# Optimization experiments

Measured on AMD Instinct MI355X. Metric: run time of the kernel, lower is better.

## Reference

```python
import jax, jax.numpy as jnp
import numpy as np


def setup_inputs() -> dict:
    key = jax.random.key(0)
    k1, k2 = jax.random.split(key)
    B, D, K = 8192, 4096, 16
    x = jax.random.normal(k1, (B, D), dtype=jnp.float32)
    # kaiming_uniform_(a=sqrt(5)) on [K, D]: bound = sqrt(6/((1+5)*fan_in)) = 1/sqrt(D)
    bound = 1.0 / np.sqrt(D)
    w = jax.random.uniform(k2, (K, D), dtype=jnp.float32, minval=-bound, maxval=bound)
    return {"x": x, "w": w}


def reference(x, w):
    # z[b,d] = x[b,d] * (1 + sum_{i=1..k} w[i-1,d] * x[b,(d+i) mod D])
    k = w.shape[0]
    acc = jnp.ones_like(x)
    for i in range(1, k + 1):
        acc = acc + w[i - 1][None, :] * jnp.roll(x, -i, axis=1)
    return x * acc
```

## Files before the change

kernel.cpp:

```cpp
#include <hip/hip_runtime.h>


#define D 4096
#define DG 1024
#define K 16
#define TPB 256
#define TILE_B 8
#define ROW_F4 260
#define ROW_F (ROW_F4 * 4)

__global__ __launch_bounds__(TPB) void quad_enhancer_kernel(
    const float* __restrict__ x, const float* __restrict__ w,
    float* __restrict__ out) {
  __shared__ float lds[TILE_B * ROW_F];

  const int tid = threadIdx.x;
  const int cg0 = blockIdx.x * TPB;
  const int cg = cg0 + tid;
  const int b0 = blockIdx.y * TILE_B;

  const float4* x4 = (const float4*)x;

#pragma unroll
  for (int r = 0; r < TILE_B; ++r) {
    const float4* gptr = &x4[(size_t)(b0 + r) * DG + cg];
    float* lptr = &lds[r * ROW_F + tid * 4];
    __builtin_amdgcn_global_load_lds(
        (const __attribute__((address_space(1))) void*)gptr,
        (__attribute__((address_space(3))) void*)lptr, 16, 0, 0);
  }
  float4 halo;
  int hr = 0, hj = 0;
  if (tid < TILE_B * 4) {
    hr = tid >> 2;
    hj = tid & 3;
    halo = x4[(size_t)(b0 + hr) * DG + ((cg0 + 256 + hj) & (DG - 1))];
  }

  const float4* w4 = (const float4*)w;
  float4 wv[K];
#pragma unroll
  for (int i = 0; i < K; ++i) wv[i] = w4[i * DG + cg];

  if (tid < TILE_B * 4) {
    *(float4*)&lds[hr * ROW_F + (256 + hj) * 4] = halo;
  }
  __syncthreads();

  float4* out4 = (float4*)out;
#pragma unroll 2
  for (int r = 0; r < TILE_B; ++r) {
    const float4* lrow = (const float4*)&lds[r * ROW_F];
    float xs[20];
#pragma unroll
    for (int j = 0; j < 5; ++j) {
      float4 v = lrow[tid + j];
      xs[4 * j + 0] = v.x;
      xs[4 * j + 1] = v.y;
      xs[4 * j + 2] = v.z;
      xs[4 * j + 3] = v.w;
    }
    float ax = 1.0f, ay = 1.0f, az = 1.0f, aw = 1.0f;
#pragma unroll
    for (int i = 0; i < K; ++i) {
      ax = fmaf(wv[i].x, xs[i + 1], ax);
      ay = fmaf(wv[i].y, xs[i + 2], ay);
      az = fmaf(wv[i].z, xs[i + 3], az);
      aw = fmaf(wv[i].w, xs[i + 4], aw);
    }
    float4 o;
    o.x = xs[0] * ax;
    o.y = xs[1] * ay;
    o.z = xs[2] * az;
    o.w = xs[3] * aw;
    out4[(size_t)(b0 + r) * DG + cg] = o;
  }
}

extern "C" void kernel_launch(void* const* d_in, const int* in_sizes, int n_in,
                              void* d_out, int out_size, void* d_ws, size_t ws_size,
                              hipStream_t stream) {
  const float* x = (const float*)d_in[0];
  const float* w = (const float*)d_in[1];
  float* out = (float*)d_out;
  const int B = in_sizes[0] / D;

  dim3 grid(DG / TPB, B / TILE_B);
  quad_enhancer_kernel<<<grid, TPB, 0, stream>>>(x, w, out);
}
```

Before: 235.7 us.

## Double-buffer LDS tiles in a persistent row loop to overlap loads with compute

Each block now walks 8 tiles of 4 rows using two LDS buffers. It prefetches the next tile with global_load_lds while computing the current one. The weights are loaded once per block and reused across 32 rows instead of 8, and the grid shrinks to 4x256 blocks. This adds a barrier per tile and hardcodes B=8192 in the launch, and with fewer blocks there is less parallelism available to hide latency.

```diff
diff --git a/kernel.cpp b/kernel.cpp
--- a/kernel.cpp
+++ b/kernel.cpp
@@ -5,75 +5,101 @@
 #define DG 1024
 #define K 16
 #define TPB 256
-#define TILE_B 8
+#define TILE_B 4
+#define NTILES 8
 #define ROW_F4 260
 #define ROW_F (ROW_F4 * 4)
 
 __global__ __launch_bounds__(TPB) void quad_enhancer_kernel(
     const float* __restrict__ x, const float* __restrict__ w,
     float* __restrict__ out) {
-  __shared__ float lds[TILE_B * ROW_F];
+  __shared__ float lds[2][TILE_B * ROW_F];
 
   const int tid = threadIdx.x;
   const int cg0 = blockIdx.x * TPB;
   const int cg = cg0 + tid;
-  const int b0 = blockIdx.y * TILE_B;
+  const float4* x4 = (const float4*)x;
+  const float4* w4 = (const float4*)w;
+  float4* out4 = (float4*)out;
 
-  const float4* x4 = (const float4*)x;
-
+  int b0 = blockIdx.y * (TILE_B * NTILES);
+  {
+    float4 h0;
+    if (tid < TILE_B * 4) {
+      h0 = x4[(size_t)(b0 + (tid >> 2)) * DG + ((cg0 + 256 + (tid & 3)) & (DG - 1))];
+    }
 #pragma unroll
-  for (int r = 0; r < TILE_B; ++r) {
-    const float4* gptr = &x4[(size_t)(b0 + r) * DG + cg];
-    float* lptr = &lds[r * ROW_F + tid * 4];
-    __builtin_amdgcn_global_load_lds(
-        (const __attribute__((address_space(1))) void*)gptr,
-        (__attribute__((address_space(3))) void*)lptr, 16, 0, 0);
-  }
-  float4 halo;
-  int hr = 0, hj = 0;
-  if (tid < TILE_B * 4) {
-    hr = tid >> 2;
-    hj = tid & 3;
-    halo = x4[(size_t)(b0 + hr) * DG + ((cg0 + 256 + hj) & (DG - 1))];
+    for (int r = 0; r < TILE_B; ++r) {
+      __builtin_amdgcn_global_load_lds(
+          (const __attribute__((address_space(1))) void*)&x4[(size_t)(b0 + r) * DG + cg],
+          (__attribute__((address_space(3))) void*)&lds[0][r * ROW_F + tid * 4],
+          16, 0, 0);
+    }
+    if (tid < TILE_B * 4) {
+      *(float4*)&lds[0][(tid >> 2) * ROW_F + (256 + (tid & 3)) * 4] = h0;
+    }
   }
 
-  const float4* w4 = (const float4*)w;
   float4 wv[K];
 #pragma unroll
   for (int i = 0; i < K; ++i) wv[i] = w4[i * DG + cg];
 
-  if (tid < TILE_B * 4) {
-    *(float4*)&lds[hr * ROW_F + (256 + hj) * 4] = halo;
-  }
   __syncthreads();
 
-  float4* out4 = (float4*)out;
-#pragma unroll 2
-  for (int r = 0; r < TILE_B; ++r) {
-    const float4* lrow = (const float4*)&lds[r * ROW_F];
-    float xs[20];
+#pragma unroll 1
+  for (int t = 0; t < NTILES; ++t) {
+    const int cur = t & 1;
+    const int nb0 = b0 + TILE_B;
+
+    float4 nhalo;
+    if (t + 1 < NTILES) {
+      if (tid < TILE_B * 4) {
+        nhalo = x4[(size_t)(nb0 + (tid >> 2)) * DG + ((cg0 + 256 + (tid & 3)) & (DG - 1))];
+      }
 #pragma unroll
-    for (int j = 0; j < 5; ++j) {
-      float4 v = lrow[tid + j];
-      xs[4 * j + 0] = v.x;
-      xs[4 * j + 1] = v.y;
-      xs[4 * j + 2] = v.z;
-      xs[4 * j + 3] = v.w;
+      for (int r = 0; r < TILE_B; ++r) {
+        __builtin_amdgcn_global_load_lds(
+            (const __attribute__((address_space(1))) void*)&x4[(size_t)(nb0 + r) * DG + cg],
+            (__attribute__((address_space(3))) void*)&lds[cur ^ 1][r * ROW_F + tid * 4],
+            16, 0, 0);
+      }
     }
-    float ax = 1.0f, ay = 1.0f, az = 1.0f, aw = 1.0f;
+
 #pragma unroll
-    for (int i = 0; i < K; ++i) {
-      ax = fmaf(wv[i].x, xs[i + 1], ax);
-      ay = fmaf(wv[i].y, xs[i + 2], ay);
-      az = fmaf(wv[i].z, xs[i + 3], az);
-      aw = fmaf(wv[i].w, xs[i + 4], aw);
+    for (int r = 0; r < TILE_B; ++r) {
+      const float4* lrow = (const float4*)&lds[cur][r * ROW_F];
+      float xs[20];
+#pragma unroll
+      for (int j = 0; j < 5; ++j) {
+        float4 v = lrow[tid + j];
+        xs[4 * j + 0] = v.x;
+        xs[4 * j + 1] = v.y;
+        xs[4 * j + 2] = v.z;
+        xs[4 * j + 3] = v.w;
+      }
+      float ax = 1.0f, ay = 1.0f, az = 1.0f, aw = 1.0f;
+#pragma unroll
+      for (int i = 0; i < K; ++i) {
+        ax = fmaf(wv[i].x, xs[i + 1], ax);
+        ay = fmaf(wv[i].y, xs[i + 2], ay);
+        az = fmaf(wv[i].z, xs[i + 3], az);
+        aw = fmaf(wv[i].w, xs[i + 4], aw);
+      }
+      float4 o;
+      o.x = xs[0] * ax;
+      o.y = xs[1] * ay;
+      o.z = xs[2] * az;
+      o.w = xs[3] * aw;
+      out4[(size_t)(b0 + r) * DG + cg] = o;
     }
-    float4 o;
-    o.x = xs[0] * ax;
-    o.y = xs[1] * ay;
-    o.z = xs[2] * az;
-    o.w = xs[3] * aw;
-    out4[(size_t)(b0 + r) * DG + cg] = o;
+
+    if (t + 1 < NTILES) {
+      if (tid < TILE_B * 4) {
+        *(float4*)&lds[cur ^ 1][(tid >> 2) * ROW_F + (256 + (tid & 3)) * 4] = nhalo;
+      }
+    }
+    __syncthreads();
+    b0 = nb0;
   }
 }
 
@@ -83,8 +109,7 @@
   const float* x = (const float*)d_in[0];
   const float* w = (const float*)d_in[1];
   float* out = (float*)d_out;
-  const int B = in_sizes[0] / D;
 
-  dim3 grid(DG / TPB, B / TILE_B);
+  dim3 grid(DG / TPB, 8192 / (TILE_B * NTILES));
   quad_enhancer_kernel<<<grid, TPB, 0, stream>>>(x, w, out);
 }
```

After: 244.2 us. 1.04x slower.
